# Optimization experiments

Measured on AMD Instinct MI355X. Metric: run time of the kernel, lower is better.

The kernel has to match this reference:

```python
import jax, jax.numpy as jnp
import numpy as np

ROUTE_NUM = 3
EPS = 1e-8


def squash(s):
    # s: [bs, J, d2]; squash along last dim
    sq = jnp.sum(s * s, axis=-1, keepdims=True)
    return (sq / (1.0 + sq)) * s / jnp.sqrt(sq + EPS)


def setup_inputs() -> dict:
    key = jax.random.key(0)
    k1, k2, k3 = jax.random.split(key, 3)
    bs, in_dim, s1 = 64, 256, 16
    out_dim, J = 32, 64           # J = num_out_caps (as_final_output)
    I = s1 * s1                   # num_in_caps = 256
    x = jax.random.normal(k1, (bs, in_dim, s1, s1), dtype=jnp.float32)
    b_init = jax.random.uniform(k2, (bs, J, I), dtype=jnp.float32)
    W = jax.random.normal(k3, (out_dim * J, in_dim), dtype=jnp.float32) * 0.05
    Wb = jnp.zeros((out_dim * J,), dtype=jnp.float32)
    return {"x": x, "b_init": b_init, "W": W, "Wb": Wb}


def reference(x, b_init, W, Wb):
    bs = x.shape[0]
    J, I = b_init.shape[1], b_init.shape[2]
    d2 = W.shape[0] // J
    # 1x1 conv == per-pixel GEMM: [bs, OUT, s1, s1]
    pred = jnp.einsum('oi,bihw->bohw', W, x) + Wb[None, :, None, None]
    # [bs, J, d2, I] -> [bs, I, J, d2]
    pred = pred.reshape(bs, J, d2, I).transpose(0, 3, 1, 2)
    b = b_init
    v = None
    for _ in range(ROUTE_NUM):
        c = jax.nn.softmax(b, axis=1)                  # softmax over out-caps J
        s = jnp.einsum('bji,bijd->bjd', c, pred)       # weighted sum over in-caps
        v = squash(s)                                  # [bs, J, d2]
        db = jax.lax.stop_gradient(jnp.einsum('bjd,bijd->bji', v, pred))
        b = b + db
    return v
```

## Files before the change

### kernel.cpp

```cpp
#include <hip/hip_runtime.h>
#include <hip/hip_bf16.h>

#define BS    64
#define KDIM  256
#define ICAP  256
#define JCAP  64
#define D2    32
#define OUTD  2048
#define NPART 16

typedef short bf16x8 __attribute__((ext_vector_type(8)));
typedef float f32x4  __attribute__((ext_vector_type(4)));

static __device__ __forceinline__ float bf2f(unsigned u16) {
  union { unsigned u; float f; } v; v.u = u16 << 16; return v.f;
}
static __device__ __forceinline__ unsigned short f2bf(float x) {
  union { float f; unsigned u; } v; v.f = x;
  unsigned r = v.u + 0x7fffu + ((v.u >> 16) & 1u);
  return (unsigned short)(r >> 16);
}
static __device__ __forceinline__ void unpack8(uint4 u, float* f) {
  f[0] = bf2f(u.x & 0xffffu); f[1] = bf2f(u.x >> 16);
  f[2] = bf2f(u.y & 0xffffu); f[3] = bf2f(u.y >> 16);
  f[4] = bf2f(u.z & 0xffffu); f[5] = bf2f(u.z >> 16);
  f[6] = bf2f(u.w & 0xffffu); f[7] = bf2f(u.w >> 16);
}
static __device__ __forceinline__ void gl_lds16(const unsigned short* g,
                                                unsigned short* l) {
  __builtin_amdgcn_global_load_lds(
      (const __attribute__((address_space(1))) unsigned int*)g,
      (__attribute__((address_space(3))) unsigned int*)l, 16, 0, 0);
}

__global__ __launch_bounds__(256) void prep(
    const float* __restrict__ W, const float* __restrict__ x,
    const float* __restrict__ Binit,
    unsigned short* __restrict__ Wbf, unsigned short* __restrict__ xT,
    unsigned short* __restrict__ c0)
{
  __shared__ union {
    float Ls[64][65];
    float Bs[64][68];
  } sm;
  const int t   = threadIdx.x;
  const int blk = blockIdx.x;

  if (blk < 256) {
    const int g = blk * 256 + t;
    const float* s = W + (size_t)g * 8;
    f32x4 a = *(const f32x4*)s;
    f32x4 b = *(const f32x4*)(s + 4);
    uint4 o;
    o.x = (unsigned)f2bf(a.x) | ((unsigned)f2bf(a.y) << 16);
    o.y = (unsigned)f2bf(a.z) | ((unsigned)f2bf(a.w) << 16);
    o.z = (unsigned)f2bf(b.x) | ((unsigned)f2bf(b.y) << 16);
    o.w = (unsigned)f2bf(b.z) | ((unsigned)f2bf(b.w) << 16);
    *(uint4*)(Wbf + (size_t)g * 8) = o;
  } else if (blk < 1280) {
    const int bid = blk - 256;
    const int i0  = (bid & 3) * 64;
    const int k0  = ((bid >> 2) & 3) * 64;
    const int b   = bid >> 4;
    for (int it = 0; it < 4; ++it) {
      const int k  = it * 16 + (t >> 4);
      const int i4 = (t & 15) * 4;
      f32x4 v = *(const f32x4*)(x + ((size_t)(b * KDIM + k0 + k) * ICAP) + i0 + i4);
      sm.Ls[k][i4 + 0] = v.x; sm.Ls[k][i4 + 1] = v.y;
      sm.Ls[k][i4 + 2] = v.z; sm.Ls[k][i4 + 3] = v.w;
    }
    __syncthreads();
    const int i  = t >> 2;
    const int kc = (t & 3) * 16;
    unsigned pk[8];
    for (int q = 0; q < 8; ++q) {
      float lo = sm.Ls[kc + 2 * q][i];
      float hi = sm.Ls[kc + 2 * q + 1][i];
      pk[q] = (unsigned)f2bf(lo) | ((unsigned)f2bf(hi) << 16);
    }
    unsigned short* dst = xT + ((size_t)(b * ICAP + i0 + i) * KDIM) + k0 + kc;
    uint4 s0; s0.x = pk[0]; s0.y = pk[1]; s0.z = pk[2]; s0.w = pk[3];
    uint4 s1; s1.x = pk[4]; s1.y = pk[5]; s1.z = pk[6]; s1.w = pk[7];
    *(uint4*)dst       = s0;
    *(uint4*)(dst + 8) = s1;
  } else {
    const int bid = blk - 1280;
    const int b   = bid >> 2;
    const int q   = bid & 3;
    {
      const int j  = t >> 2;
      const int c4 = (t & 3) * 16;
      const float* src = Binit + ((size_t)(b * JCAP + j) * ICAP) + q * 64 + c4;
      for (int r = 0; r < 4; ++r) {
        f32x4 v = *(const f32x4*)(src + r * 4);
        *(f32x4*)&sm.Bs[j][c4 + r * 4] = v;
      }
    }
    __syncthreads();
    if (t < 64) {
      const int ii = t;
      float m = -3.0e38f;
      for (int j = 0; j < 64; ++j) m = fmaxf(m, sm.Bs[j][ii]);
      float se = 0.f;
      for (int j = 0; j < 64; ++j) se += __expf(sm.Bs[j][ii] - m);
      const float inv = 1.0f / se;
      unsigned short* dst = c0 + ((size_t)(b * ICAP + q * 64 + ii) * JCAP);
      for (int qq = 0; qq < 8; ++qq) {
        unsigned pk[4];
        for (int h = 0; h < 4; ++h) {
          float lo = __expf(sm.Bs[qq * 8 + 2 * h][ii] - m) * inv;
          float hi = __expf(sm.Bs[qq * 8 + 2 * h + 1][ii] - m) * inv;
          pk[h] = (unsigned)f2bf(lo) | ((unsigned)f2bf(hi) << 16);
        }
        uint4 s; s.x = pk[0]; s.y = pk[1]; s.z = pk[2]; s.w = pk[3];
        *(uint4*)(dst + qq * 8) = s;
      }
    }
  }
}

__global__ __launch_bounds__(256) void gemm_pred(
    const unsigned short* __restrict__ Wbf,
    const unsigned short* __restrict__ xT,
    const float* __restrict__ Wb,
    const unsigned short* __restrict__ c0,
    unsigned short* __restrict__ P,
    float* __restrict__ s0part)
{
  __shared__ union {
    unsigned short AB[2][128][64];
    struct {
      unsigned short C[128][136];
      unsigned short c0t[128][4];
    } ep;
  } sm;

  const int tid = threadIdx.x;
  const int b   = blockIdx.z;
  const int o0  = blockIdx.x * 128;
  const int i0  = blockIdx.y * 128;
  const int l   = tid & 63;
  const int m   = l & 15;
  const int w   = tid >> 6;
  const int wo  = (w & 1) * 64;
  const int wi  = (w >> 1) * 64;

  const int srow = l >> 3;
  const int gch  = (l & 7) ^ srow;

  f32x4 acc[4][4];
  for (int a = 0; a < 4; ++a)
    for (int c = 0; c < 4; ++c) acc[a][c] = (f32x4){0.f, 0.f, 0.f, 0.f};

  for (int r = 0; r < 4; ++r) {
    const int k0 = r * 64;
    __syncthreads();
    for (int c = 0; c < 4; ++c) {
      const int q   = w * 4 + c;
      const int row = q * 8 + srow;
      gl_lds16(Wbf + (size_t)(o0 + row) * KDIM + k0 + gch * 8,
               &sm.AB[0][q * 8][0]);
      gl_lds16(xT + ((size_t)(b * ICAP + i0 + row) * KDIM) + k0 + gch * 8,
               &sm.AB[1][q * 8][0]);
    }
    __syncthreads();
    for (int ks = 0; ks < 2; ++ks) {
      const int clog = ks * 4 + (l >> 4);
      bf16x8 af[4], bfg[4];
      for (int ti = 0; ti < 4; ++ti) {
        const int row = wo + 16 * ti + m;
        af[ti] = *(const bf16x8*)&sm.AB[0][row][(clog ^ (m & 7)) * 8];
      }
      for (int tj = 0; tj < 4; ++tj) {
        const int row = wi + 16 * tj + m;
        bfg[tj] = *(const bf16x8*)&sm.AB[1][row][(clog ^ (m & 7)) * 8];
      }
      for (int ti = 0; ti < 4; ++ti)
        for (int tj = 0; tj < 4; ++tj)
          acc[ti][tj] = __builtin_amdgcn_mfma_f32_16x16x32_bf16(
              af[ti], bfg[tj], acc[ti][tj], 0, 0, 0);
    }
  }

  __syncthreads();
  {
    const int q4 = (l >> 4) * 4;
    for (int ti = 0; ti < 4; ++ti) {
      const int ob = wo + 16 * ti + q4;
      f32x4 wb4 = *(const f32x4*)(Wb + o0 + ob);
      for (int tj = 0; tj < 4; ++tj) {
        const int ii = wi + 16 * tj + m;
        f32x4 a = acc[ti][tj];
        uint2 pk;
        pk.x = (unsigned)f2bf(a.x + wb4.x) | ((unsigned)f2bf(a.y + wb4.y) << 16);
        pk.y = (unsigned)f2bf(a.z + wb4.z) | ((unsigned)f2bf(a.w + wb4.w) << 16);
        *(uint2*)&sm.ep.C[ii][ob] = pk;
      }
    }
  }
  if (tid < 128) {
    const int j0 = blockIdx.x * 4;
    uint2 v = *(const uint2*)(c0 + ((size_t)(b * ICAP + i0 + tid) * JCAP) + j0);
    *(uint2*)&sm.ep.c0t[tid][0] = v;
  }
  __syncthreads();
  for (int rr = 0; rr < 8; ++rr) {
    const int id  = rr * 256 + tid;
    const int row = id >> 4;
    const int seg = id & 15;
    uint4 v = *(const uint4*)&sm.ep.C[row][seg * 8];
    *(uint4*)(P + ((size_t)(b * ICAP + i0 + row) * OUTD) + o0 + seg * 8) = v;
  }
  {
    const int oc = tid & 127;
    const int h  = tid >> 7;
    const int jj = oc >> 5;
    float s = 0.f;
    for (int ii = 0; ii < 64; ++ii) {
      const int i = h * 64 + ii;
      s += bf2f(sm.ep.C[i][oc]) * bf2f(sm.ep.c0t[i][jj]);
    }
    const int p = blockIdx.y * 2 + h;
    s0part[((size_t)(b * 4 + p) * OUTD) + o0 + oc] = s;
  }
}

__global__ __launch_bounds__(256) void route_fused(
    const unsigned short* __restrict__ P,
    const float* __restrict__ Binit,
    float* __restrict__ B1,
    const float* __restrict__ part_in,
    const int npart_in,
    float* __restrict__ part_out,
    const int pass)
{
  __shared__ union {
    float Vs[2112];
    float Ps[4][2112];
  } sm;

  const int tid = threadIdx.x;
  const int l   = tid & 63;
  const int w   = tid >> 6;
  const int b   = blockIdx.x >> 4;
  const int g   = blockIdx.x & 15;

  {
    const float* base = part_in + (size_t)b * npart_in * OUTD + tid * 8;
    float s[8] = {0.f,0.f,0.f,0.f,0.f,0.f,0.f,0.f};
    for (int p = 0; p < npart_in; ++p) {
      f32x4 a = *(const f32x4*)(base + (size_t)p * OUTD);
      f32x4 c = *(const f32x4*)(base + (size_t)p * OUTD + 4);
      s[0] += a.x; s[1] += a.y; s[2] += a.z; s[3] += a.w;
      s[4] += c.x; s[5] += c.y; s[6] += c.z; s[7] += c.w;
    }
    float sq = 0.f;
    for (int c = 0; c < 8; ++c) sq += s[c] * s[c];
    sq += __shfl_xor(sq, 1, 64);
    sq += __shfl_xor(sq, 2, 64);
    float scale = (sq / (1.0f + sq)) / sqrtf(sq + 1e-8f);
    const int j  = tid >> 2;
    const int d0 = (tid & 3) * 8;
    for (int c = 0; c < 8; ++c) sm.Vs[j * 33 + d0 + c] = scale * s[c];
  }
  __syncthreads();
  float vv[32];
  for (int k = 0; k < 32; ++k) vv[k] = sm.Vs[l * 33 + k];

  const int i0 = g * 16 + w * 4;
  float bold[4];
  if (pass == 1) {
    f32x4 t = *(const f32x4*)(Binit + (size_t)(b * JCAP + l) * ICAP + i0);
    bold[0] = t.x; bold[1] = t.y; bold[2] = t.z; bold[3] = t.w;
  } else {
    for (int ii = 0; ii < 4; ++ii)
      bold[ii] = B1[((size_t)(b * ICAP + i0 + ii)) * JCAP + l];
  }

  float sacc[32];
  for (int k = 0; k < 32; ++k) sacc[k] = 0.f;

  const unsigned short* pbase = P + ((size_t)(b * ICAP + i0) * OUTD) + l * D2;
  uint4 ubuf[2][4];
  for (int q = 0; q < 4; ++q) ubuf[0][q] = *(const uint4*)(pbase + q * 8);
  for (int q = 0; q < 4; ++q) ubuf[1][q] = *(const uint4*)(pbase + OUTD + q * 8);

#pragma unroll
  for (int ii = 0; ii < 4; ++ii) {
    uint4 cur[4];
    for (int q = 0; q < 4; ++q) cur[q] = ubuf[ii & 1][q];
    if (ii + 2 < 4)
      for (int q = 0; q < 4; ++q)
        ubuf[ii & 1][q] = *(const uint4*)(pbase + (size_t)(ii + 2) * OUTD + q * 8);

    float db = 0.f;
    for (int q = 0; q < 4; ++q) {
      float ps[8]; unpack8(cur[q], ps);
      for (int k = 0; k < 8; ++k) db += ps[k] * vv[q * 8 + k];
    }
    float bnew = bold[ii] + db;
    if (pass == 1) B1[((size_t)(b * ICAP + i0 + ii)) * JCAP + l] = bnew;

    float mx = bnew;
    for (int off = 1; off < 64; off <<= 1) mx = fmaxf(mx, __shfl_xor(mx, off, 64));
    float e = __expf(bnew - mx);
    float se = e;
    for (int off = 1; off < 64; off <<= 1) se += __shfl_xor(se, off, 64);
    float c = e / se;
    for (int q = 0; q < 4; ++q) {
      float ps[8]; unpack8(cur[q], ps);
      for (int k = 0; k < 8; ++k) sacc[q * 8 + k] += c * ps[k];
    }
  }

  __syncthreads();
  for (int k = 0; k < 32; ++k) sm.Ps[w][l * 33 + k] = sacc[k];
  __syncthreads();

  {
    const int o0 = tid * 8;
    float s[8];
    for (int c = 0; c < 8; ++c) {
      const int o = o0 + c, j = o >> 5, d = o & 31, idx = j * 33 + d;
      s[c] = sm.Ps[0][idx] + sm.Ps[1][idx] + sm.Ps[2][idx] + sm.Ps[3][idx];
    }
    float* dst = part_out + ((size_t)(b * NPART + g)) * OUTD + o0;
    f32x4 t0 = {s[0], s[1], s[2], s[3]};
    f32x4 t1 = {s[4], s[5], s[6], s[7]};
    *(f32x4*)dst       = t0;
    *(f32x4*)(dst + 4) = t1;
  }
}

__global__ __launch_bounds__(256) void squash_final(
    const float* __restrict__ part,
    float* __restrict__ outp)
{
  const int tid = threadIdx.x;
  const int b   = blockIdx.x;
  const float* base = part + (size_t)b * NPART * OUTD + tid * 8;
  float s[8] = {0.f,0.f,0.f,0.f,0.f,0.f,0.f,0.f};
  for (int p = 0; p < NPART; ++p) {
    f32x4 a = *(const f32x4*)(base + (size_t)p * OUTD);
    f32x4 c = *(const f32x4*)(base + (size_t)p * OUTD + 4);
    s[0] += a.x; s[1] += a.y; s[2] += a.z; s[3] += a.w;
    s[4] += c.x; s[5] += c.y; s[6] += c.z; s[7] += c.w;
  }
  float sq = 0.f;
  for (int c = 0; c < 8; ++c) sq += s[c] * s[c];
  sq += __shfl_xor(sq, 1, 64);
  sq += __shfl_xor(sq, 2, 64);
  float scale = (sq / (1.0f + sq)) / sqrtf(sq + 1e-8f);
  float* dst = outp + (size_t)b * OUTD + tid * 8;
  f32x4 t0 = {scale*s[0], scale*s[1], scale*s[2], scale*s[3]};
  f32x4 t1 = {scale*s[4], scale*s[5], scale*s[6], scale*s[7]};
  *(f32x4*)dst       = t0;
  *(f32x4*)(dst + 4) = t1;
}

extern "C" void kernel_launch(void* const* d_in, const int* in_sizes, int n_in,
                              void* d_out, int out_size, void* d_ws, size_t ws_size,
                              hipStream_t stream) {
  const float* x  = (const float*)d_in[0];
  const float* bi = (const float*)d_in[1];
  const float* W  = (const float*)d_in[2];
  const float* Wb = (const float*)d_in[3];
  float* out = (float*)d_out;

  char* ws = (char*)d_ws;
  const size_t MiB = 1024 * 1024;
  unsigned short* P        = (unsigned short*)ws;
  unsigned short* xT       = (unsigned short*)(ws + 64 * MiB);
  float*          partial1 = (float*)(ws + 64 * MiB);
  unsigned short* Wbf      = (unsigned short*)(ws + 72 * MiB);
  unsigned short* c0       = (unsigned short*)(ws + 73 * MiB);
  float*          s0part   = (float*)(ws + 75 * MiB);
  float*          partial2 = (float*)(ws + 72 * MiB);
  float* B1                = (float*)(ws + 80 * MiB);

  prep<<<dim3(1536), 256, 0, stream>>>(W, x, bi, Wbf, xT, c0);
  gemm_pred<<<dim3(16, 2, 64), 256, 0, stream>>>(Wbf, xT, Wb, c0, P, s0part);
  route_fused<<<dim3(1024), 256, 0, stream>>>(P, bi, B1, s0part, 4, partial1, 1);
  route_fused<<<dim3(1024), 256, 0, stream>>>(P, bi, B1, partial1, NPART, partial2, 2);
  squash_final<<<dim3(64), 256, 0, stream>>>(partial2, out);
}
```

Before: 154.4 us.

## Split squash into separate kernels, halve GEMM epilogue LDS, raise route occupancy

The GEMM epilogue now stages the output tile in two halves, halving the shared C buffer, and writes eight s0 partials per batch instead of four. The squash of partial sums moves out of route_fused into a standalone squash_v kernel run before each routing pass, so route blocks read a precomputed V instead of each re-reducing the partials. route_fused gets launch_bounds(256,4), a smaller LDS footprint, and simpler non-double-buffered P loads. The aim is less redundant reduction work and higher occupancy, at the cost of two extra kernel launches, extra epilogue syncs, and weaker load prefetching.

```diff
diff --git a/kernel.cpp b/kernel.cpp
--- a/kernel.cpp
+++ b/kernel.cpp
@@ -130,7 +130,7 @@
   __shared__ union {
     unsigned short AB[2][128][64];
     struct {
-      unsigned short C[128][136];
+      unsigned short C[64][136];
       unsigned short c0t[128][4];
     } ep;
   } sm;
@@ -143,7 +143,6 @@
   const int m   = l & 15;
   const int w   = tid >> 6;
   const int wo  = (w & 1) * 64;
-  const int wi  = (w >> 1) * 64;
 
   const int srow = l >> 3;
   const int gch  = (l & 7) ^ srow;
@@ -172,7 +171,7 @@
         af[ti] = *(const bf16x8*)&sm.AB[0][row][(clog ^ (m & 7)) * 8];
       }
       for (int tj = 0; tj < 4; ++tj) {
-        const int row = wi + 16 * tj + m;
+        const int row = (w >> 1) * 64 + 16 * tj + m;
         bfg[tj] = *(const bf16x8*)&sm.AB[1][row][(clog ^ (m & 7)) * 8];
       }
       for (int ti = 0; ti < 4; ++ti)
@@ -183,61 +182,88 @@
   }
 
   __syncthreads();
-  {
-    const int q4 = (l >> 4) * 4;
-    for (int ti = 0; ti < 4; ++ti) {
-      const int ob = wo + 16 * ti + q4;
-      f32x4 wb4 = *(const f32x4*)(Wb + o0 + ob);
-      for (int tj = 0; tj < 4; ++tj) {
-        const int ii = wi + 16 * tj + m;
-        f32x4 a = acc[ti][tj];
-        uint2 pk;
-        pk.x = (unsigned)f2bf(a.x + wb4.x) | ((unsigned)f2bf(a.y + wb4.y) << 16);
-        pk.y = (unsigned)f2bf(a.z + wb4.z) | ((unsigned)f2bf(a.w + wb4.w) << 16);
-        *(uint2*)&sm.ep.C[ii][ob] = pk;
-      }
-    }
-  }
   if (tid < 128) {
     const int j0 = blockIdx.x * 4;
     uint2 v = *(const uint2*)(c0 + ((size_t)(b * ICAP + i0 + tid) * JCAP) + j0);
     *(uint2*)&sm.ep.c0t[tid][0] = v;
   }
-  __syncthreads();
-  for (int rr = 0; rr < 8; ++rr) {
-    const int id  = rr * 256 + tid;
-    const int row = id >> 4;
-    const int seg = id & 15;
-    uint4 v = *(const uint4*)&sm.ep.C[row][seg * 8];
-    *(uint4*)(P + ((size_t)(b * ICAP + i0 + row) * OUTD) + o0 + seg * 8) = v;
-  }
-  {
-    const int oc = tid & 127;
-    const int h  = tid >> 7;
-    const int jj = oc >> 5;
-    float s = 0.f;
-    for (int ii = 0; ii < 64; ++ii) {
-      const int i = h * 64 + ii;
-      s += bf2f(sm.ep.C[i][oc]) * bf2f(sm.ep.c0t[i][jj]);
-    }
-    const int p = blockIdx.y * 2 + h;
-    s0part[((size_t)(b * 4 + p) * OUTD) + o0 + oc] = s;
-  }
-}
-
-__global__ __launch_bounds__(256) void route_fused(
+
+  for (int half = 0; half < 2; ++half) {
+    __syncthreads();
+    if ((w >> 1) == half) {
+      const int q4 = (l >> 4) * 4;
+      for (int ti = 0; ti < 4; ++ti) {
+        const int ob = wo + 16 * ti + q4;
+        f32x4 wb4 = *(const f32x4*)(Wb + o0 + ob);
+        for (int tj = 0; tj < 4; ++tj) {
+          const int ii = 16 * tj + m;
+          f32x4 a = acc[ti][tj];
+          uint2 pk;
+          pk.x = (unsigned)f2bf(a.x + wb4.x) | ((unsigned)f2bf(a.y + wb4.y) << 16);
+          pk.y = (unsigned)f2bf(a.z + wb4.z) | ((unsigned)f2bf(a.w + wb4.w) << 16);
+          *(uint2*)&sm.ep.C[ii][ob] = pk;
+        }
+      }
+    }
+    __syncthreads();
+    for (int rr = 0; rr < 4; ++rr) {
+      const int id  = rr * 256 + tid;
+      const int row = id >> 4;
+      const int seg = id & 15;
+      uint4 v = *(const uint4*)&sm.ep.C[row][seg * 8];
+      *(uint4*)(P + ((size_t)(b * ICAP + i0 + half * 64 + row) * OUTD) + o0 + seg * 8) = v;
+    }
+    {
+      const int oc = tid & 127;
+      const int q  = tid >> 7;
+      const int jj = oc >> 5;
+      float s = 0.f;
+      for (int r2 = 0; r2 < 32; ++r2) {
+        const int il = q * 32 + r2;
+        s += bf2f(sm.ep.C[il][oc]) * bf2f(sm.ep.c0t[half * 64 + il][jj]);
+      }
+      const int p = blockIdx.y * 4 + half * 2 + q;
+      s0part[((size_t)(b * 8 + p) * OUTD) + o0 + oc] = s;
+    }
+  }
+}
+
+__global__ __launch_bounds__(256) void squash_v(
+    const float* __restrict__ part,
+    const int npart,
+    float* __restrict__ dst)
+{
+  const int tid = threadIdx.x;
+  const int b   = blockIdx.x;
+  const float* base = part + (size_t)b * npart * OUTD + tid * 8;
+  float s[8] = {0.f,0.f,0.f,0.f,0.f,0.f,0.f,0.f};
+  for (int p = 0; p < npart; ++p) {
+    f32x4 a = *(const f32x4*)(base + (size_t)p * OUTD);
+    f32x4 c = *(const f32x4*)(base + (size_t)p * OUTD + 4);
+    s[0] += a.x; s[1] += a.y; s[2] += a.z; s[3] += a.w;
+    s[4] += c.x; s[5] += c.y; s[6] += c.z; s[7] += c.w;
+  }
+  float sq = 0.f;
+  for (int c = 0; c < 8; ++c) sq += s[c] * s[c];
+  sq += __shfl_xor(sq, 1, 64);
+  sq += __shfl_xor(sq, 2, 64);
+  float scale = (sq / (1.0f + sq)) / sqrtf(sq + 1e-8f);
+  float* d = dst + (size_t)b * OUTD + tid * 8;
+  f32x4 t0 = {scale*s[0], scale*s[1], scale*s[2], scale*s[3]};
+  f32x4 t1 = {scale*s[4], scale*s[5], scale*s[6], scale*s[7]};
+  *(f32x4*)d       = t0;
+  *(f32x4*)(d + 4) = t1;
+}
+
+__global__ __launch_bounds__(256, 4) void route_fused(
     const unsigned short* __restrict__ P,
     const float* __restrict__ Binit,
     float* __restrict__ B1,
-    const float* __restrict__ part_in,
-    const int npart_in,
+    const float* __restrict__ Vin,
     float* __restrict__ part_out,
     const int pass)
 {
-  __shared__ union {
-    float Vs[2112];
-    float Ps[4][2112];
-  } sm;
+  __shared__ float Ps[4][2112];
 
   const int tid = threadIdx.x;
   const int l   = tid & 63;
@@ -245,27 +271,14 @@
   const int b   = blockIdx.x >> 4;
   const int g   = blockIdx.x & 15;
 
+  float vv[32];
   {
-    const float* base = part_in + (size_t)b * npart_in * OUTD + tid * 8;
-    float s[8] = {0.f,0.f,0.f,0.f,0.f,0.f,0.f,0.f};
-    for (int p = 0; p < npart_in; ++p) {
-      f32x4 a = *(const f32x4*)(base + (size_t)p * OUTD);
-      f32x4 c = *(const f32x4*)(base + (size_t)p * OUTD + 4);
-      s[0] += a.x; s[1] += a.y; s[2] += a.z; s[3] += a.w;
-      s[4] += c.x; s[5] += c.y; s[6] += c.z; s[7] += c.w;
-    }
-    float sq = 0.f;
-    for (int c = 0; c < 8; ++c) sq += s[c] * s[c];
-    sq += __shfl_xor(sq, 1, 64);
-    sq += __shfl_xor(sq, 2, 64);
-    float scale = (sq / (1.0f + sq)) / sqrtf(sq + 1e-8f);
-    const int j  = tid >> 2;
-    const int d0 = (tid & 3) * 8;
-    for (int c = 0; c < 8; ++c) sm.Vs[j * 33 + d0 + c] = scale * s[c];
-  }
-  __syncthreads();
-  float vv[32];
-  for (int k = 0; k < 32; ++k) vv[k] = sm.Vs[l * 33 + k];
+    const float* vp = Vin + (size_t)b * OUTD + l * D2;
+    for (int q = 0; q < 8; ++q) {
+      f32x4 t = *(const f32x4*)(vp + q * 4);
+      vv[q*4+0] = t.x; vv[q*4+1] = t.y; vv[q*4+2] = t.z; vv[q*4+3] = t.w;
+    }
+  }
 
   const int i0 = g * 16 + w * 4;
   float bold[4];
@@ -281,23 +294,18 @@
   for (int k = 0; k < 32; ++k) sacc[k] = 0.f;
 
   const unsigned short* pbase = P + ((size_t)(b * ICAP + i0) * OUTD) + l * D2;
-  uint4 ubuf[2][4];
-  for (int q = 0; q < 4; ++q) ubuf[0][q] = *(const uint4*)(pbase + q * 8);
-  for (int q = 0; q < 4; ++q) ubuf[1][q] = *(const uint4*)(pbase + OUTD + q * 8);
 
 #pragma unroll
   for (int ii = 0; ii < 4; ++ii) {
-    uint4 cur[4];
-    for (int q = 0; q < 4; ++q) cur[q] = ubuf[ii & 1][q];
-    if (ii + 2 < 4)
-      for (int q = 0; q < 4; ++q)
-        ubuf[ii & 1][q] = *(const uint4*)(pbase + (size_t)(ii + 2) * OUTD + q * 8);
+    uint4 u0 = *(const uint4*)(pbase + (size_t)ii * OUTD);
+    uint4 u1 = *(const uint4*)(pbase + (size_t)ii * OUTD + 8);
+    uint4 u2 = *(const uint4*)(pbase + (size_t)ii * OUTD + 16);
+    uint4 u3 = *(const uint4*)(pbase + (size_t)ii * OUTD + 24);
+    float ps[32];
+    unpack8(u0, ps); unpack8(u1, ps + 8); unpack8(u2, ps + 16); unpack8(u3, ps + 24);
 
     float db = 0.f;
-    for (int q = 0; q < 4; ++q) {
-      float ps[8]; unpack8(cur[q], ps);
-      for (int k = 0; k < 8; ++k) db += ps[k] * vv[q * 8 + k];
-    }
+    for (int k = 0; k < 32; ++k) db += ps[k] * vv[k];
     float bnew = bold[ii] + db;
     if (pass == 1) B1[((size_t)(b * ICAP + i0 + ii)) * JCAP + l] = bnew;
 
@@ -307,14 +315,10 @@
     float se = e;
     for (int off = 1; off < 64; off <<= 1) se += __shfl_xor(se, off, 64);
     float c = e / se;
-    for (int q = 0; q < 4; ++q) {
-      float ps[8]; unpack8(cur[q], ps);
-      for (int k = 0; k < 8; ++k) sacc[q * 8 + k] += c * ps[k];
-    }
-  }
-
-  __syncthreads();
-  for (int k = 0; k < 32; ++k) sm.Ps[w][l * 33 + k] = sacc[k];
+    for (int k = 0; k < 32; ++k) sacc[k] += c * ps[k];
+  }
+
+  for (int k = 0; k < 32; ++k) Ps[w][l * 33 + k] = sacc[k];
   __syncthreads();
 
   {
@@ -322,7 +326,7 @@
     float s[8];
     for (int c = 0; c < 8; ++c) {
       const int o = o0 + c, j = o >> 5, d = o & 31, idx = j * 33 + d;
-      s[c] = sm.Ps[0][idx] + sm.Ps[1][idx] + sm.Ps[2][idx] + sm.Ps[3][idx];
+      s[c] = Ps[0][idx] + Ps[1][idx] + Ps[2][idx] + Ps[3][idx];
     }
     float* dst = part_out + ((size_t)(b * NPART + g)) * OUTD + o0;
     f32x4 t0 = {s[0], s[1], s[2], s[3]};
@@ -330,32 +334,6 @@
     *(f32x4*)dst       = t0;
     *(f32x4*)(dst + 4) = t1;
   }
-}
-
-__global__ __launch_bounds__(256) void squash_final(
-    const float* __restrict__ part,
-    float* __restrict__ outp)
-{
-  const int tid = threadIdx.x;
-  const int b   = blockIdx.x;
-  const float* base = part + (size_t)b * NPART * OUTD + tid * 8;
-  float s[8] = {0.f,0.f,0.f,0.f,0.f,0.f,0.f,0.f};
-  for (int p = 0; p < NPART; ++p) {
-    f32x4 a = *(const f32x4*)(base + (size_t)p * OUTD);
-    f32x4 c = *(const f32x4*)(base + (size_t)p * OUTD + 4);
-    s[0] += a.x; s[1] += a.y; s[2] += a.z; s[3] += a.w;
-    s[4] += c.x; s[5] += c.y; s[6] += c.z; s[7] += c.w;
-  }
-  float sq = 0.f;
-  for (int c = 0; c < 8; ++c) sq += s[c] * s[c];
-  sq += __shfl_xor(sq, 1, 64);
-  sq += __shfl_xor(sq, 2, 64);
-  float scale = (sq / (1.0f + sq)) / sqrtf(sq + 1e-8f);
-  float* dst = outp + (size_t)b * OUTD + tid * 8;
-  f32x4 t0 = {scale*s[0], scale*s[1], scale*s[2], scale*s[3]};
-  f32x4 t1 = {scale*s[4], scale*s[5], scale*s[6], scale*s[7]};
-  *(f32x4*)dst       = t0;
-  *(f32x4*)(dst + 4) = t1;
 }
 
 extern "C" void kernel_launch(void* const* d_in, const int* in_sizes, int n_in,
@@ -372,15 +350,19 @@
   unsigned short* P        = (unsigned short*)ws;
   unsigned short* xT       = (unsigned short*)(ws + 64 * MiB);
   float*          partial1 = (float*)(ws + 64 * MiB);
-  unsigned short* Wbf      = (unsigned short*)(ws + 72 * MiB);
-  unsigned short* c0       = (unsigned short*)(ws + 73 * MiB);
-  float*          s0part   = (float*)(ws + 75 * MiB);
+  float*          s0part   = (float*)(ws + 72 * MiB);
+  unsigned short* Wbf      = (unsigned short*)(ws + 76 * MiB);
+  unsigned short* c0       = (unsigned short*)(ws + 77 * MiB);
   float*          partial2 = (float*)(ws + 72 * MiB);
   float* B1                = (float*)(ws + 80 * MiB);
+  float* V1                = (float*)(ws + 84 * MiB);
+  float* V2                = (float*)(ws + 84 * MiB + 512 * 1024);
 
   prep<<<dim3(1536), 256, 0, stream>>>(W, x, bi, Wbf, xT, c0);
   gemm_pred<<<dim3(16, 2, 64), 256, 0, stream>>>(Wbf, xT, Wb, c0, P, s0part);
-  route_fused<<<dim3(1024), 256, 0, stream>>>(P, bi, B1, s0part, 4, partial1, 1);
-  route_fused<<<dim3(1024), 256, 0, stream>>>(P, bi, B1, partial1, NPART, partial2, 2);
-  squash_final<<<dim3(64), 256, 0, stream>>>(partial2, out);
-}
+  squash_v<<<dim3(64), 256, 0, stream>>>(s0part, 8, V1);
+  route_fused<<<dim3(1024), 256, 0, stream>>>(P, bi, B1, V1, partial1, 1);
+  squash_v<<<dim3(64), 256, 0, stream>>>(partial1, NPART, V2);
+  route_fused<<<dim3(1024), 256, 0, stream>>>(P, bi, B1, V2, partial2, 2);
+  squash_v<<<dim3(64), 256, 0, stream>>>(partial2, NPART, out);
+}
```

Result: slower. 199.8 us (+29.4%).
